# Kernel optimization log

Measured on AMD Instinct MI355X. Metric: run time of the kernel, lower is better.

## Reference

```python
import jax, jax.numpy as jnp
import numpy as np


def _nearest(img, cy, cx):
    # PyTorch F.grid_sample(mode='nearest', align_corners=False, padding_mode='zeros').
    # img: [B,C,H,W]; cy,cx: [B,N] normalized coords in [-1,1] (cy->H axis, cx->W axis).
    B, C, H, W = img.shape
    iy = jnp.rint((cy + 1.0) * H / 2.0 - 0.5)  # unnormalize then nearbyint
    ix = jnp.rint((cx + 1.0) * W / 2.0 - 0.5)
    valid = (iy >= 0) & (iy < H) & (ix >= 0) & (ix < W)
    flat = (jnp.clip(iy, 0, H - 1).astype(jnp.int32) * W
            + jnp.clip(ix, 0, W - 1).astype(jnp.int32))  # [B,N]
    g = jnp.take_along_axis(img.reshape(B, C, H * W), flat[:, None, :], axis=2)  # [B,C,N]
    g = jnp.where(valid[:, None, :], g, 0.0)
    return g.transpose(0, 2, 1)  # [B,N,C]


def setup_inputs() -> dict:
    key = jax.random.key(0)
    ks = jax.random.split(key, 16)
    B, N = 2, 16384
    h, w = 64, 64       # LR feat / lr_guide resolution
    H, W = 256, 256     # HR guide resolution
    Cf, Cg = 128, 128   # feat_dim, guide_dim
    inp = {
        'feat': jax.random.normal(ks[0], (B, Cf, h, w), jnp.float32),
        'coord': jax.random.uniform(ks[1], (B, N, 2), jnp.float32) * 2.0 - 1.0,
        'hr_guide': jax.random.normal(ks[2], (B, Cg, H, W), jnp.float32),
        'lr_guide': jax.random.normal(ks[3], (B, Cg, h, w), jnp.float32),
    }
    dims = [386, 1024, 512, 256, 128, 2]  # imnet_in_dim -> hidden_list -> out_dim
    for i in range(5):
        fan_in, fan_out = dims[i], dims[i + 1]
        scale = np.sqrt(2.0 / fan_in).astype(np.float32)
        inp[f'W{i}'] = jax.random.normal(ks[4 + i], (fan_out, fan_in), jnp.float32) * scale
        inp[f'b{i}'] = jnp.zeros((fan_out,), jnp.float32)
    return inp


def reference(feat, coord, hr_guide, lr_guide, W0, b0, W1, b1, W2, b2, W3, b3, W4, b4):
    b, c, h, w = feat.shape
    # make_coord((h,w), flatten=False).permute(2,0,1): channel 0 = y (h axis), 1 = x (w axis)
    ys = -1.0 + 2.0 * (jnp.arange(h, dtype=jnp.float32) + 0.5) / h
    xs = -1.0 + 2.0 * (jnp.arange(w, dtype=jnp.float32) + 0.5) / w
    fc = jnp.stack([jnp.broadcast_to(ys[:, None], (h, w)),
                    jnp.broadcast_to(xs[None, :], (h, w))], 0)[None]  # [1,2,h,w]
    fc = jnp.broadcast_to(fc, (b, 2, h, w))

    # coord.flip(-1) as grid -> grid x = coord[...,1] (W axis), grid y = coord[...,0] (H axis)
    q_guide_hr = _nearest(hr_guide, coord[..., 0], coord[..., 1])  # [B,N,Cg]

    # 4 offsets (vx,vy) in [-1,1]x[-1,1], scaled by rx=1/h, ry=1/w (loop order of torch code)
    offs = jnp.array([[-1., -1.], [-1., 1.], [1., -1.], [1., 1.]], jnp.float32)
    offs = offs * jnp.array([1.0 / h, 1.0 / w], jnp.float32)
    cK = coord[None] + offs[:, None, None, :]  # [4,B,N,2]

    samp = jax.vmap(_nearest, in_axes=(None, 0, 0))
    q_feat = samp(feat, cK[..., 0], cK[..., 1])      # [4,B,N,Cf]
    q_coord = samp(fc, cK[..., 0], cK[..., 1])       # [4,B,N,2]
    q_lr = samp(lr_guide, cK[..., 0], cK[..., 1])    # [4,B,N,Cg]

    rel = (coord[None] - q_coord) * jnp.array([float(h), float(w)], jnp.float32)  # [4,B,N,2]
    qg_hr = jnp.broadcast_to(q_guide_hr[None], q_lr.shape)
    inp = jnp.concatenate([q_feat, qg_hr, qg_hr - q_lr, rel], axis=-1)  # [4,B,N,386]

    x = inp
    for Wl, bl in ((W0, b0), (W1, b1), (W2, b2), (W3, b3)):
        x = jax.nn.relu(x @ Wl.T + bl)
    preds = x @ W4.T + b4                      # [4,B,N,2]
    preds = jnp.moveaxis(preds, 0, -1)         # [B,N,2,4]
    wgt = jax.nn.softmax(preds[:, :, 1, :], axis=-1)
    return jnp.sum(preds[:, :, 0, :] * wgt, axis=-1, keepdims=True)  # [B,N,1]
```

## Files before the change

### kernel.cpp

```cpp
#include <hip/hip_runtime.h>
#include <cstdint>

typedef __attribute__((ext_vector_type(8))) _Float16 half8;
typedef __attribute__((ext_vector_type(16))) float   f32x16;

#define BN 2
#define NN 16384
#define FH 64
#define FW 64
#define GH 256
#define GW 256
#define CC 128
#define M_TOTAL (4*BN*NN)
#define MROWS 64
#define NBLK (M_TOTAL/MROWS)

#define SX  456
#define SC  264
#define S2H 520
#define S3  264
#define S4  136
#define OFF_HC 29184
#define OFF_H3 33280
#define LDS_ELEMS 50176

#define MFMA(a,b,c) __builtin_amdgcn_mfma_f32_32x32x16_f16((a),(b),(c),0,0,0)

static __device__ __forceinline__ f32x16 zero16() {
  f32x16 z;
#pragma unroll
  for (int i = 0; i < 16; ++i) z[i] = 0.f;
  return z;
}
static __device__ __forceinline__ half8 zero8() {
  half8 z;
#pragma unroll
  for (int e = 0; e < 8; ++e) z[e] = (_Float16)0.f;
  return z;
}

__global__ void pack_w(const float* __restrict__ wsrc, _Float16* __restrict__ out,
                       int NT, int K, int KT) {
  int idx = blockIdx.x * 256 + threadIdx.x;
  int total = NT * KT * 64;
  if (idx >= total) return;
  int l = idx & 63;
  int t = idx >> 6;
  int kt = t % KT;
  int jt = t / KT;
  int row = jt * 32 + (l & 31);
  int k0 = kt * 16 + (l >> 5) * 8;
  _Float16* o = out + (size_t)idx * 8;
#pragma unroll
  for (int e = 0; e < 8; ++e) {
    int k = k0 + e;
    float v = (k < K) ? wsrc[(size_t)row * K + k] : 0.f;
    o[e] = (_Float16)v;
  }
}

__global__ void transpose_to_hwc(const float* __restrict__ in, _Float16* __restrict__ out,
                                 int C, int HH, int WW) {
  __shared__ float tile[32][33];
  const int xt = blockIdx.x, ct = blockIdx.y;
  const int bb = blockIdx.z / HH, y = blockIdx.z % HH;
  const int tx = threadIdx.x, ty = threadIdx.y;
  const int x0 = xt * 32, c0 = ct * 32;
#pragma unroll
  for (int i = 0; i < 4; ++i) {
    int c = c0 + ty + i * 8;
    tile[ty + i * 8][tx] = in[((size_t)(bb * C + c) * HH + y) * WW + x0 + tx];
  }
  __syncthreads();
#pragma unroll
  for (int i = 0; i < 4; ++i) {
    int x = x0 + ty + i * 8;
    out[((size_t)(bb * HH + y) * WW + x) * C + c0 + tx] = (_Float16)tile[tx][ty + i * 8];
  }
}

template<bool RELU>
static __device__ __forceinline__ void store_tile(const f32x16 acc, _Float16* lout, int ldo,
                                                  int row0, int col0,
                                                  const float* __restrict__ biasBase, int lane) {
  const int m = row0 + (lane & 31);
  const int s4 = (lane >> 5) * 4;
  _Float16* rp = lout + (size_t)m * ldo + col0 + s4;
  const float* bp = biasBase + s4;
#pragma unroll
  for (int g = 0; g < 4; ++g) {
    float4 bv = *(const float4*)(bp + 8 * g);
    union { _Float16 h[4]; unsigned long long u; } pk;
#pragma unroll
    for (int e = 0; e < 4; ++e) {
      float v = acc[4 * g + e] + ((const float*)&bv)[e];
      if (RELU) v = fmaxf(v, 0.f);
      pk.h[e] = (_Float16)v;
    }
    *(unsigned long long*)(rp + 8 * g) = pk.u;
  }
}

__global__ __launch_bounds__(512, 2) void jiif_main(
    const float* __restrict__ coord,
    const _Float16* __restrict__ featT, const _Float16* __restrict__ hrT,
    const _Float16* __restrict__ lrT,
    const _Float16* __restrict__ W0p, const _Float16* __restrict__ W1p,
    const _Float16* __restrict__ W2p, const _Float16* __restrict__ W3p,
    const float* __restrict__ b0, const float* __restrict__ b1,
    const float* __restrict__ b2, const float* __restrict__ b3,
    const float* __restrict__ W4, const float* __restrict__ b4,
    float* __restrict__ preds) {
  extern __shared__ _Float16 lds[];
  const int tid = threadIdx.x;
  const int w = tid >> 6, lane = tid & 63;
  const int m0 = blockIdx.x * MROWS;
  _Float16* X   = lds;
  _Float16* Hc  = lds + OFF_HC;
  _Float16* H2r = lds;
  _Float16* H3r = lds + OFF_H3;
  _Float16* H4r = lds;

  {
    const int r = tid >> 3;
    const int g = tid & 7;
    const int row = m0 + r;
    const int n = row & (NN - 1);
    const int bb = (row >> 14) & (BN - 1);
    const int k = row >> 15;
    const float c0 = coord[((size_t)bb * NN + n) * 2 + 0];
    const float c1 = coord[((size_t)bb * NN + n) * 2 + 1];
    const float cy = c0 + ((k < 2) ? -1.f : 1.f) * (1.f / FH);
    const float cx = c1 + ((k & 1) ? 1.f : -1.f) * (1.f / FW);
    const float fy = rintf((cy + 1.f) * (FH * 0.5f) - 0.5f);
    const float fx = rintf((cx + 1.f) * (FW * 0.5f) - 0.5f);
    const bool vF = (fy >= 0.f) && (fy < (float)FH) && (fx >= 0.f) && (fx < (float)FW);
    const int iy = max(0, min(FH - 1, (int)fy));
    const int ix = max(0, min(FW - 1, (int)fx));
    const float gy = rintf((c0 + 1.f) * (GH * 0.5f) - 0.5f);
    const float gx = rintf((c1 + 1.f) * (GW * 0.5f) - 0.5f);
    const bool vH = (gy >= 0.f) && (gy < (float)GH) && (gx >= 0.f) && (gx < (float)GW);
    const int jy = max(0, min(GH - 1, (int)gy));
    const int jx = max(0, min(GW - 1, (int)gx));
    const _Float16* fp = featT + (size_t)((bb * FH + iy) * FW + ix) * CC;
    const _Float16* lp = lrT  + (size_t)((bb * FH + iy) * FW + ix) * CC;
    const _Float16* hp = hrT  + (size_t)((bb * GH + jy) * GW + jx) * CC;
    _Float16* xr = X + (size_t)r * SX;
#pragma unroll
    for (int t = 0; t < 2; ++t) {
      const int c8 = g * 16 + t * 8;
      half8 fv = vF ? *(const half8*)(fp + c8) : zero8();
      half8 lv = vF ? *(const half8*)(lp + c8) : zero8();
      half8 hv = vH ? *(const half8*)(hp + c8) : zero8();
      *(half8*)(xr + c8) = fv;
      *(half8*)(xr + CC + c8) = hv;
      half8 dv = hv - lv;
      *(half8*)(xr + 2 * CC + c8) = dv;
    }
    *(unsigned long long*)(xr + 384 + g * 8) = 0ull;
    *(unsigned long long*)(xr + 384 + g * 8 + 4) = 0ull;
    if (g == 0) {
      const float qc0 = vF ? (-1.f + (float)(2 * iy + 1) * (1.f / FH)) : 0.f;
      const float qc1 = vF ? (-1.f + (float)(2 * ix + 1) * (1.f / FW)) : 0.f;
      xr[384] = (_Float16)((c0 - qc0) * (float)FH);
      xr[385] = (_Float16)((c1 - qc1) * (float)FW);
    }
  }
  __syncthreads();

  const int m31 = lane & 31;
  const int s8 = (lane >> 5) * 8;
  const _Float16* xb0 = X + (size_t)m31 * SX + s8;
  const _Float16* xb1 = X + (size_t)(32 + m31) * SX + s8;

  f32x16 a2_00 = zero16(), a2_01 = zero16(), a2_10 = zero16(), a2_11 = zero16();
#pragma unroll 1
  for (int c = 0; c < 4; ++c) {
    f32x16 a0lo = zero16(), a0hi = zero16();
    {
      const _Float16* wb = W0p + ((size_t)(c * 8 + w) * 28 * 64 + lane) * 8;
#pragma unroll 1
      for (int t = 0; t < 4; ++t) {
        half8 A[7], B0[7], B1[7];
#pragma unroll
        for (int i = 0; i < 7; ++i) {
          const int kt = t * 7 + i;
          A[i]  = *(const half8*)(wb + kt * 512);
          B0[i] = *(const half8*)(xb0 + kt * 16);
          B1[i] = *(const half8*)(xb1 + kt * 16);
        }
        __builtin_amdgcn_s_setprio(1);
#pragma unroll
        for (int i = 0; i < 7; ++i) {
          a0lo = MFMA(A[i], B0[i], a0lo);
          a0hi = MFMA(A[i], B1[i], a0hi);
        }
        __builtin_amdgcn_s_setprio(0);
      }
    }
    store_tile<true>(a0lo, Hc, SC, 0,  w * 32, b0 + c * 256 + w * 32, lane);
    store_tile<true>(a0hi, Hc, SC, 32, w * 32, b0 + c * 256 + w * 32, lane);
    __syncthreads();
    {
      const _Float16* w1a = W1p + ((size_t)(w * 64 + c * 16) * 64 + lane) * 8;
      const _Float16* w1b = W1p + ((size_t)((w + 8) * 64 + c * 16) * 64 + lane) * 8;
      const _Float16* hb0 = Hc + (size_t)m31 * SC + s8;
      const _Float16* hb1 = Hc + (size_t)(32 + m31) * SC + s8;
#pragma unroll 1
      for (int t = 0; t < 4; ++t) {
        half8 A0[4], A1[4], B0[4], B1[4];
#pragma unroll
        for (int i = 0; i < 4; ++i) {
          const int kt = t * 4 + i;
          A0[i] = *(const half8*)(w1a + kt * 512);
          A1[i] = *(const half8*)(w1b + kt * 512);
          B0[i] = *(const half8*)(hb0 + kt * 16);
          B1[i] = *(const half8*)(hb1 + kt * 16);
        }
        __builtin_amdgcn_s_setprio(1);
#pragma unroll
        for (int i = 0; i < 4; ++i) {
          a2_00 = MFMA(A0[i], B0[i], a2_00);
          a2_01 = MFMA(A0[i], B1[i], a2_01);
          a2_10 = MFMA(A1[i], B0[i], a2_10);
          a2_11 = MFMA(A1[i], B1[i], a2_11);
        }
        __builtin_amdgcn_s_setprio(0);
      }
    }
    __syncthreads();
  }

  store_tile<true>(a2_00, H2r, S2H, 0,  w * 32,       b1 + w * 32,       lane);
  store_tile<true>(a2_01, H2r, S2H, 32, w * 32,       b1 + w * 32,       lane);
  store_tile<true>(a2_10, H2r, S2H, 0,  256 + w * 32, b1 + 256 + w * 32, lane);
  store_tile<true>(a2_11, H2r, S2H, 32, 256 + w * 32, b1 + 256 + w * 32, lane);
  __syncthreads();

  {
    f32x16 a3lo = zero16(), a3hi = zero16();
    const _Float16* wb = W2p + ((size_t)(w * 32) * 64 + lane) * 8;
    const _Float16* hb0 = H2r + (size_t)m31 * S2H + s8;
    const _Float16* hb1 = H2r + (size_t)(32 + m31) * S2H + s8;
#pragma unroll 1
    for (int t = 0; t < 4; ++t) {
      half8 A[8], B0[8], B1[8];
#pragma unroll
      for (int i = 0; i < 8; ++i) {
        const int kt = t * 8 + i;
        A[i]  = *(const half8*)(wb + kt * 512);
        B0[i] = *(const half8*)(hb0 + kt * 16);
        B1[i] = *(const half8*)(hb1 + kt * 16);
      }
      __builtin_amdgcn_s_setprio(1);
#pragma unroll
      for (int i = 0; i < 8; ++i) {
        a3lo = MFMA(A[i], B0[i], a3lo);
        a3hi = MFMA(A[i], B1[i], a3hi);
      }
      __builtin_amdgcn_s_setprio(0);
    }
    store_tile<true>(a3lo, H3r, S3, 0,  w * 32, b2 + w * 32, lane);
    store_tile<true>(a3hi, H3r, S3, 32, w * 32, b2 + w * 32, lane);
  }
  __syncthreads();

  {
    const int j3 = w & 3, mts = w >> 2;
    f32x16 a4 = zero16();
    const _Float16* wb = W3p + ((size_t)(j3 * 16) * 64 + lane) * 8;
    const _Float16* hb = H3r + (size_t)(mts * 32 + m31) * S3 + s8;
#pragma unroll 1
    for (int t = 0; t < 2; ++t) {
      half8 A[8], B[8];
#pragma unroll
      for (int i = 0; i < 8; ++i) {
        const int kt = t * 8 + i;
        A[i] = *(const half8*)(wb + kt * 512);
        B[i] = *(const half8*)(hb + kt * 16);
      }
      __builtin_amdgcn_s_setprio(1);
#pragma unroll
      for (int i = 0; i < 8; ++i) a4 = MFMA(A[i], B[i], a4);
      __builtin_amdgcn_s_setprio(0);
    }
    store_tile<true>(a4, H4r, S4, mts * 32, j3 * 32, b3 + j3 * 32, lane);
  }
  __syncthreads();

  {
    const int m = tid >> 3;
    const int sub = tid & 7;
    const int j = sub & 1;
    const int q = sub >> 1;
    const _Float16* h4 = H4r + (size_t)m * S4 + q * 32;
    const float* w4 = W4 + j * CC + q * 32;
    float s = 0.f;
#pragma unroll
    for (int cc = 0; cc < 32; ++cc) s += (float)h4[cc] * w4[cc];
    s += __shfl_xor(s, 2);
    s += __shfl_xor(s, 4);
    if (q == 0) preds[(size_t)(m0 + m) * 2 + j] = s + b4[j];
  }
}

__global__ void jiif_combine(const float* __restrict__ preds, float* __restrict__ out) {
  const int i = blockIdx.x * 256 + threadIdx.x;
  if (i >= BN * NN) return;
  float p0[4], p1[4];
#pragma unroll
  for (int k = 0; k < 4; ++k) {
    p0[k] = preds[((size_t)k * BN * NN + i) * 2 + 0];
    p1[k] = preds[((size_t)k * BN * NN + i) * 2 + 1];
  }
  float mx = fmaxf(fmaxf(p1[0], p1[1]), fmaxf(p1[2], p1[3]));
  float se = 0.f, so = 0.f;
#pragma unroll
  for (int k = 0; k < 4; ++k) {
    float e = expf(p1[k] - mx);
    se += e;
    so += p0[k] * e;
  }
  out[i] = so / se;
}

extern "C" void kernel_launch(void* const* d_in, const int* in_sizes, int n_in,
                              void* d_out, int out_size, void* d_ws, size_t ws_size,
                              hipStream_t stream) {
  const float* feat  = (const float*)d_in[0];
  const float* coord = (const float*)d_in[1];
  const float* hr    = (const float*)d_in[2];
  const float* lr    = (const float*)d_in[3];
  const float* W0 = (const float*)d_in[4];  const float* b0 = (const float*)d_in[5];
  const float* W1 = (const float*)d_in[6];  const float* b1 = (const float*)d_in[7];
  const float* W2 = (const float*)d_in[8];  const float* b2 = (const float*)d_in[9];
  const float* W3 = (const float*)d_in[10]; const float* b3 = (const float*)d_in[11];
  const float* W4 = (const float*)d_in[12]; const float* b4 = (const float*)d_in[13];

  char* ws = (char*)d_ws;
  _Float16* W0p   = (_Float16*)(ws + 0);
  _Float16* W1p   = (_Float16*)(ws + 917504);
  _Float16* W2p   = (_Float16*)(ws + 1966080);
  _Float16* W3p   = (_Float16*)(ws + 2228224);
  _Float16* featT = (_Float16*)(ws + 2293760);
  _Float16* hrT   = (_Float16*)(ws + 4390912);
  _Float16* lrT   = (_Float16*)(ws + 37945344);
  float* preds    = (float*)(ws + 40042496);
  if (ws_size < 41091072) return;

  pack_w<<<224, 256, 0, stream>>>(W0, W0p, 32, 386, 28);
  pack_w<<<256, 256, 0, stream>>>(W1, W1p, 16, 1024, 64);
  pack_w<<<64,  256, 0, stream>>>(W2, W2p, 8, 512, 32);
  pack_w<<<16,  256, 0, stream>>>(W3, W3p, 4, 256, 16);

  transpose_to_hwc<<<dim3(2, 4, 128), dim3(32, 8), 0, stream>>>(feat, featT, CC, FH, FW);
  transpose_to_hwc<<<dim3(8, 4, 512), dim3(32, 8), 0, stream>>>(hr,   hrT,   CC, GH, GW);
  transpose_to_hwc<<<dim3(2, 4, 128), dim3(32, 8), 0, stream>>>(lr,   lrT,   CC, FH, FW);

  (void)hipFuncSetAttribute((const void*)jiif_main,
                            hipFuncAttributeMaxDynamicSharedMemorySize, LDS_ELEMS * 2);
  jiif_main<<<NBLK, 512, LDS_ELEMS * 2, stream>>>(
      coord, featT, hrT, lrT, W0p, W1p, W2p, W3p, b0, b1, b2, b3, W4, b4, preds);

  jiif_combine<<<(BN * NN + 255) / 256, 256, 0, stream>>>(preds, (float*)d_out);
}
```

Measured before the change: 373.1 us.

## Double-buffer operand loads across MFMA chunks with sched barriers in all GEMM layers

Replaces the per-chunk load-then-compute loops in each MLP layer with fully unrolled ping-pong register buffers. The next chunk's weight (global) and activation (LDS) fragments load while the current chunk's MFMAs run, and sched_barrier keeps the compiler from reordering them. The goal is to hide global and LDS load latency behind matrix math. In exchange it holds two buffer sets in registers, which raises VGPR pressure and may lower occupancy.

```diff
diff --git a/kernel.cpp b/kernel.cpp
--- a/kernel.cpp
+++ b/kernel.cpp
@@ -37,6 +37,76 @@
 #pragma unroll
   for (int e = 0; e < 8; ++e) z[e] = (_Float16)0.f;
   return z;
+}
+
+
+static __device__ __forceinline__ void ld_ab2(half8 (&A)[4], half8 (&B0)[4], half8 (&B1)[4],
+    const _Float16* wb, const _Float16* xb0, const _Float16* xb1, int t) {
+#pragma unroll
+  for (int i = 0; i < 4; ++i) {
+    const int kt = t * 4 + i;
+    A[i]  = *(const half8*)(wb  + kt * 512);
+    B0[i] = *(const half8*)(xb0 + kt * 16);
+    B1[i] = *(const half8*)(xb1 + kt * 16);
+  }
+}
+static __device__ __forceinline__ void mm_ab2(f32x16& lo, f32x16& hi,
+    const half8 (&A)[4], const half8 (&B0)[4], const half8 (&B1)[4]) {
+  __builtin_amdgcn_sched_barrier(0);
+  __builtin_amdgcn_s_setprio(1);
+#pragma unroll
+  for (int i = 0; i < 4; ++i) {
+    lo = MFMA(A[i], B0[i], lo);
+    hi = MFMA(A[i], B1[i], hi);
+  }
+  __builtin_amdgcn_s_setprio(0);
+  __builtin_amdgcn_sched_barrier(0);
+}
+
+static __device__ __forceinline__ void ld_a2b2(half8 (&A0)[4], half8 (&A1)[4],
+    half8 (&B0)[4], half8 (&B1)[4],
+    const _Float16* wa, const _Float16* wb, const _Float16* xb0, const _Float16* xb1, int t) {
+#pragma unroll
+  for (int i = 0; i < 4; ++i) {
+    const int kt = t * 4 + i;
+    A0[i] = *(const half8*)(wa + kt * 512);
+    A1[i] = *(const half8*)(wb + kt * 512);
+    B0[i] = *(const half8*)(xb0 + kt * 16);
+    B1[i] = *(const half8*)(xb1 + kt * 16);
+  }
+}
+static __device__ __forceinline__ void mm_a2b2(f32x16& a00, f32x16& a01, f32x16& a10, f32x16& a11,
+    const half8 (&A0)[4], const half8 (&A1)[4], const half8 (&B0)[4], const half8 (&B1)[4]) {
+  __builtin_amdgcn_sched_barrier(0);
+  __builtin_amdgcn_s_setprio(1);
+#pragma unroll
+  for (int i = 0; i < 4; ++i) {
+    a00 = MFMA(A0[i], B0[i], a00);
+    a01 = MFMA(A0[i], B1[i], a01);
+    a10 = MFMA(A1[i], B0[i], a10);
+    a11 = MFMA(A1[i], B1[i], a11);
+  }
+  __builtin_amdgcn_s_setprio(0);
+  __builtin_amdgcn_sched_barrier(0);
+}
+
+static __device__ __forceinline__ void ld_ab1(half8 (&A)[4], half8 (&B)[4],
+    const _Float16* wb, const _Float16* xb, int t) {
+#pragma unroll
+  for (int i = 0; i < 4; ++i) {
+    const int kt = t * 4 + i;
+    A[i] = *(const half8*)(wb + kt * 512);
+    B[i] = *(const half8*)(xb + kt * 16);
+  }
+}
+static __device__ __forceinline__ void mm_ab1(f32x16& acc,
+    const half8 (&A)[4], const half8 (&B)[4]) {
+  __builtin_amdgcn_sched_barrier(0);
+  __builtin_amdgcn_s_setprio(1);
+#pragma unroll
+  for (int i = 0; i < 4; ++i) acc = MFMA(A[i], B[i], acc);
+  __builtin_amdgcn_s_setprio(0);
+  __builtin_amdgcn_sched_barrier(0);
 }
 
 __global__ void pack_w(const float* __restrict__ wsrc, _Float16* __restrict__ out,
@@ -179,24 +249,15 @@
     f32x16 a0lo = zero16(), a0hi = zero16();
     {
       const _Float16* wb = W0p + ((size_t)(c * 8 + w) * 28 * 64 + lane) * 8;
-#pragma unroll 1
-      for (int t = 0; t < 4; ++t) {
-        half8 A[7], B0[7], B1[7];
-#pragma unroll
-        for (int i = 0; i < 7; ++i) {
-          const int kt = t * 7 + i;
-          A[i]  = *(const half8*)(wb + kt * 512);
-          B0[i] = *(const half8*)(xb0 + kt * 16);
-          B1[i] = *(const half8*)(xb1 + kt * 16);
-        }
-        __builtin_amdgcn_s_setprio(1);
-#pragma unroll
-        for (int i = 0; i < 7; ++i) {
-          a0lo = MFMA(A[i], B0[i], a0lo);
-          a0hi = MFMA(A[i], B1[i], a0hi);
-        }
-        __builtin_amdgcn_s_setprio(0);
-      }
+      half8 sA[4], sB0[4], sB1[4], tA[4], tB0[4], tB1[4];
+      ld_ab2(sA, sB0, sB1, wb, xb0, xb1, 0);
+      ld_ab2(tA, tB0, tB1, wb, xb0, xb1, 1); mm_ab2(a0lo, a0hi, sA, sB0, sB1);
+      ld_ab2(sA, sB0, sB1, wb, xb0, xb1, 2); mm_ab2(a0lo, a0hi, tA, tB0, tB1);
+      ld_ab2(tA, tB0, tB1, wb, xb0, xb1, 3); mm_ab2(a0lo, a0hi, sA, sB0, sB1);
+      ld_ab2(sA, sB0, sB1, wb, xb0, xb1, 4); mm_ab2(a0lo, a0hi, tA, tB0, tB1);
+      ld_ab2(tA, tB0, tB1, wb, xb0, xb1, 5); mm_ab2(a0lo, a0hi, sA, sB0, sB1);
+      ld_ab2(sA, sB0, sB1, wb, xb0, xb1, 6); mm_ab2(a0lo, a0hi, tA, tB0, tB1);
+      mm_ab2(a0lo, a0hi, sA, sB0, sB1);
     }
     store_tile<true>(a0lo, Hc, SC, 0,  w * 32, b0 + c * 256 + w * 32, lane);
     store_tile<true>(a0hi, Hc, SC, 32, w * 32, b0 + c * 256 + w * 32, lane);
@@ -206,27 +267,15 @@
       const _Float16* w1b = W1p + ((size_t)((w + 8) * 64 + c * 16) * 64 + lane) * 8;
       const _Float16* hb0 = Hc + (size_t)m31 * SC + s8;
       const _Float16* hb1 = Hc + (size_t)(32 + m31) * SC + s8;
-#pragma unroll 1
-      for (int t = 0; t < 4; ++t) {
-        half8 A0[4], A1[4], B0[4], B1[4];
-#pragma unroll
-        for (int i = 0; i < 4; ++i) {
-          const int kt = t * 4 + i;
-          A0[i] = *(const half8*)(w1a + kt * 512);
-          A1[i] = *(const half8*)(w1b + kt * 512);
-          B0[i] = *(const half8*)(hb0 + kt * 16);
-          B1[i] = *(const half8*)(hb1 + kt * 16);
-        }
-        __builtin_amdgcn_s_setprio(1);
-#pragma unroll
-        for (int i = 0; i < 4; ++i) {
-          a2_00 = MFMA(A0[i], B0[i], a2_00);
-          a2_01 = MFMA(A0[i], B1[i], a2_01);
-          a2_10 = MFMA(A1[i], B0[i], a2_10);
-          a2_11 = MFMA(A1[i], B1[i], a2_11);
-        }
-        __builtin_amdgcn_s_setprio(0);
-      }
+      half8 sA0[4], sA1[4], sB0[4], sB1[4], tA0[4], tA1[4], tB0[4], tB1[4];
+      ld_a2b2(sA0, sA1, sB0, sB1, w1a, w1b, hb0, hb1, 0);
+      ld_a2b2(tA0, tA1, tB0, tB1, w1a, w1b, hb0, hb1, 1);
+      mm_a2b2(a2_00, a2_01, a2_10, a2_11, sA0, sA1, sB0, sB1);
+      ld_a2b2(sA0, sA1, sB0, sB1, w1a, w1b, hb0, hb1, 2);
+      mm_a2b2(a2_00, a2_01, a2_10, a2_11, tA0, tA1, tB0, tB1);
+      ld_a2b2(tA0, tA1, tB0, tB1, w1a, w1b, hb0, hb1, 3);
+      mm_a2b2(a2_00, a2_01, a2_10, a2_11, sA0, sA1, sB0, sB1);
+      mm_a2b2(a2_00, a2_01, a2_10, a2_11, tA0, tA1, tB0, tB1);
     }
     __syncthreads();
   }
@@ -242,24 +291,16 @@
     const _Float16* wb = W2p + ((size_t)(w * 32) * 64 + lane) * 8;
     const _Float16* hb0 = H2r + (size_t)m31 * S2H + s8;
     const _Float16* hb1 = H2r + (size_t)(32 + m31) * S2H + s8;
-#pragma unroll 1
-    for (int t = 0; t < 4; ++t) {
-      half8 A[8], B0[8], B1[8];
-#pragma unroll
-      for (int i = 0; i < 8; ++i) {
-        const int kt = t * 8 + i;
-        A[i]  = *(const half8*)(wb + kt * 512);
-        B0[i] = *(const half8*)(hb0 + kt * 16);
-        B1[i] = *(const half8*)(hb1 + kt * 16);
-      }
-      __builtin_amdgcn_s_setprio(1);
-#pragma unroll
-      for (int i = 0; i < 8; ++i) {
-        a3lo = MFMA(A[i], B0[i], a3lo);
-        a3hi = MFMA(A[i], B1[i], a3hi);
-      }
-      __builtin_amdgcn_s_setprio(0);
-    }
+    half8 sA[4], sB0[4], sB1[4], tA[4], tB0[4], tB1[4];
+    ld_ab2(sA, sB0, sB1, wb, hb0, hb1, 0);
+    ld_ab2(tA, tB0, tB1, wb, hb0, hb1, 1); mm_ab2(a3lo, a3hi, sA, sB0, sB1);
+    ld_ab2(sA, sB0, sB1, wb, hb0, hb1, 2); mm_ab2(a3lo, a3hi, tA, tB0, tB1);
+    ld_ab2(tA, tB0, tB1, wb, hb0, hb1, 3); mm_ab2(a3lo, a3hi, sA, sB0, sB1);
+    ld_ab2(sA, sB0, sB1, wb, hb0, hb1, 4); mm_ab2(a3lo, a3hi, tA, tB0, tB1);
+    ld_ab2(tA, tB0, tB1, wb, hb0, hb1, 5); mm_ab2(a3lo, a3hi, sA, sB0, sB1);
+    ld_ab2(sA, sB0, sB1, wb, hb0, hb1, 6); mm_ab2(a3lo, a3hi, tA, tB0, tB1);
+    ld_ab2(tA, tB0, tB1, wb, hb0, hb1, 7); mm_ab2(a3lo, a3hi, sA, sB0, sB1);
+    mm_ab2(a3lo, a3hi, tA, tB0, tB1);
     store_tile<true>(a3lo, H3r, S3, 0,  w * 32, b2 + w * 32, lane);
     store_tile<true>(a3hi, H3r, S3, 32, w * 32, b2 + w * 32, lane);
   }
@@ -270,20 +311,12 @@
     f32x16 a4 = zero16();
     const _Float16* wb = W3p + ((size_t)(j3 * 16) * 64 + lane) * 8;
     const _Float16* hb = H3r + (size_t)(mts * 32 + m31) * S3 + s8;
-#pragma unroll 1
-    for (int t = 0; t < 2; ++t) {
-      half8 A[8], B[8];
-#pragma unroll
-      for (int i = 0; i < 8; ++i) {
-        const int kt = t * 8 + i;
-        A[i] = *(const half8*)(wb + kt * 512);
-        B[i] = *(const half8*)(hb + kt * 16);
-      }
-      __builtin_amdgcn_s_setprio(1);
-#pragma unroll
-      for (int i = 0; i < 8; ++i) a4 = MFMA(A[i], B[i], a4);
-      __builtin_amdgcn_s_setprio(0);
-    }
+    half8 sA[4], sB[4], tA[4], tB[4];
+    ld_ab1(sA, sB, wb, hb, 0);
+    ld_ab1(tA, tB, wb, hb, 1); mm_ab1(a4, sA, sB);
+    ld_ab1(sA, sB, wb, hb, 2); mm_ab1(a4, tA, tB);
+    ld_ab1(tA, tB, wb, hb, 3); mm_ab1(a4, sA, sB);
+    mm_ab1(a4, tA, tB);
     store_tile<true>(a4, H4r, S4, mts * 32, j3 * 32, b3 + j3 * 32, lane);
   }
   __syncthreads();
```

Measured after the change: 359.4 us. 3.7% less time.

## Restructure layer0/1 into two 512-wide chunks with double-buffered register prefetch

Applied to the files above, without the earlier changes.

Layer 0 is now computed in two halves of 512 hidden units, each stored to a widened LDS buffer, instead of four 256-wide chunks. Layer 1 therefore accumulates over two large K chunks, which halves the number of block barriers. All GEMM loops now use ping-pong register buffers, so the next K-slice is loaded while the MFMAs run on the current one, with sched_barrier fencing the MFMA groups. The cost is a larger LDS footprint (about 159KB) and more registers, which may reduce occupancy.

```diff
diff --git a/kernel.cpp b/kernel.cpp
--- a/kernel.cpp
+++ b/kernel.cpp
@@ -16,13 +16,13 @@
 #define NBLK (M_TOTAL/MROWS)
 
 #define SX  456
-#define SC  264
+#define SHC 520
 #define S2H 520
 #define S3  264
 #define S4  136
 #define OFF_HC 29184
-#define OFF_H3 33280
-#define LDS_ELEMS 50176
+#define OFF_H3 62464
+#define LDS_ELEMS 79360
 
 #define MFMA(a,b,c) __builtin_amdgcn_mfma_f32_32x32x16_f16((a),(b),(c),0,0,0)
 
@@ -37,6 +37,76 @@
 #pragma unroll
   for (int e = 0; e < 8; ++e) z[e] = (_Float16)0.f;
   return z;
+}
+
+template<int NB>
+static __device__ __forceinline__ void ldA2(half8 (&A0)[NB], half8 (&A1)[NB],
+    const _Float16* wa, const _Float16* wb, int t) {
+#pragma unroll
+  for (int i = 0; i < NB; ++i) {
+    const int kt = t * NB + i;
+    A0[i] = *(const half8*)(wa + kt * 512);
+    A1[i] = *(const half8*)(wb + kt * 512);
+  }
+}
+template<int NB>
+static __device__ __forceinline__ void ldA1(half8 (&A)[NB], const _Float16* wa, int t) {
+#pragma unroll
+  for (int i = 0; i < NB; ++i) A[i] = *(const half8*)(wa + (t * NB + i) * 512);
+}
+template<int NB>
+static __device__ __forceinline__ void ldB2(half8 (&B0)[NB], half8 (&B1)[NB],
+    const _Float16* p0, const _Float16* p1, int t) {
+#pragma unroll
+  for (int i = 0; i < NB; ++i) {
+    const int kt = t * NB + i;
+    B0[i] = *(const half8*)(p0 + kt * 16);
+    B1[i] = *(const half8*)(p1 + kt * 16);
+  }
+}
+template<int NB>
+static __device__ __forceinline__ void ldB1(half8 (&B)[NB], const _Float16* p, int t) {
+#pragma unroll
+  for (int i = 0; i < NB; ++i) B[i] = *(const half8*)(p + (t * NB + i) * 16);
+}
+
+template<int NB>
+static __device__ __forceinline__ void mm_22(f32x16& a00, f32x16& a01, f32x16& a10, f32x16& a11,
+    const half8 (&A0)[NB], const half8 (&A1)[NB], const half8 (&B0)[NB], const half8 (&B1)[NB]) {
+  __builtin_amdgcn_sched_barrier(0);
+  __builtin_amdgcn_s_setprio(1);
+#pragma unroll
+  for (int i = 0; i < NB; ++i) {
+    a00 = MFMA(A0[i], B0[i], a00);
+    a01 = MFMA(A0[i], B1[i], a01);
+    a10 = MFMA(A1[i], B0[i], a10);
+    a11 = MFMA(A1[i], B1[i], a11);
+  }
+  __builtin_amdgcn_s_setprio(0);
+  __builtin_amdgcn_sched_barrier(0);
+}
+template<int NB>
+static __device__ __forceinline__ void mm_12(f32x16& lo, f32x16& hi,
+    const half8 (&A)[NB], const half8 (&B0)[NB], const half8 (&B1)[NB]) {
+  __builtin_amdgcn_sched_barrier(0);
+  __builtin_amdgcn_s_setprio(1);
+#pragma unroll
+  for (int i = 0; i < NB; ++i) {
+    lo = MFMA(A[i], B0[i], lo);
+    hi = MFMA(A[i], B1[i], hi);
+  }
+  __builtin_amdgcn_s_setprio(0);
+  __builtin_amdgcn_sched_barrier(0);
+}
+template<int NB>
+static __device__ __forceinline__ void mm_11(f32x16& acc,
+    const half8 (&A)[NB], const half8 (&B)[NB]) {
+  __builtin_amdgcn_sched_barrier(0);
+  __builtin_amdgcn_s_setprio(1);
+#pragma unroll
+  for (int i = 0; i < NB; ++i) acc = MFMA(A[i], B[i], acc);
+  __builtin_amdgcn_s_setprio(0);
+  __builtin_amdgcn_sched_barrier(0);
 }
 
 __global__ void pack_w(const float* __restrict__ wsrc, _Float16* __restrict__ out,
@@ -171,95 +241,116 @@
   const int m31 = lane & 31;
   const int s8 = (lane >> 5) * 8;
   const _Float16* xb0 = X + (size_t)m31 * SX + s8;
-  const _Float16* xb1 = X + (size_t)(32 + m31) * SX + s8;
+  const _Float16* xb1 = xb0 + 32 * SX;
+  const _Float16* hb0 = Hc + (size_t)m31 * SHC + s8;
+  const _Float16* hb1 = hb0 + 32 * SHC;
+
+  {
+    f32x16 a00 = zero16(), a01 = zero16(), a10 = zero16(), a11 = zero16();
+    const _Float16* wa = W0p + ((size_t)(2 * w) * 28 * 64 + lane) * 8;
+    const _Float16* wb = wa + 28 * 512;
+    half8 pA0[2], pA1[2], pB0[2], pB1[2], qA0[2], qA1[2], qB0[2], qB1[2];
+    ldA2<2>(pA0, pA1, wa, wb, 0); ldB2<2>(pB0, pB1, xb0, xb1, 0);
+    ldA2<2>(qA0, qA1, wa, wb, 1); ldB2<2>(qB0, qB1, xb0, xb1, 1);
+#pragma unroll 1
+    for (int u = 0; u < 6; ++u) {
+      mm_22<2>(a00, a01, a10, a11, pA0, pA1, pB0, pB1);
+      ldA2<2>(pA0, pA1, wa, wb, 2 * u + 2); ldB2<2>(pB0, pB1, xb0, xb1, 2 * u + 2);
+      mm_22<2>(a00, a01, a10, a11, qA0, qA1, qB0, qB1);
+      ldA2<2>(qA0, qA1, wa, wb, 2 * u + 3); ldB2<2>(qB0, qB1, xb0, xb1, 2 * u + 3);
+    }
+    mm_22<2>(a00, a01, a10, a11, pA0, pA1, pB0, pB1);
+    mm_22<2>(a00, a01, a10, a11, qA0, qA1, qB0, qB1);
+    store_tile<true>(a00, Hc, SHC, 0,  (2 * w) * 32,     b0 + (2 * w) * 32,     lane);
+    store_tile<true>(a01, Hc, SHC, 32, (2 * w) * 32,     b0 + (2 * w) * 32,     lane);
+    store_tile<true>(a10, Hc, SHC, 0,  (2 * w + 1) * 32, b0 + (2 * w + 1) * 32, lane);
+    store_tile<true>(a11, Hc, SHC, 32, (2 * w + 1) * 32, b0 + (2 * w + 1) * 32, lane);
+  }
+  __syncthreads();
 
   f32x16 a2_00 = zero16(), a2_01 = zero16(), a2_10 = zero16(), a2_11 = zero16();
+  const _Float16* w1a = W1p + ((size_t)(2 * w) * 64 * 64 + lane) * 8;
+  const _Float16* w1b = w1a + 64 * 512;
+  {
+    half8 sA0[4], sA1[4], sB0[4], sB1[4], tA0[4], tA1[4], tB0[4], tB1[4];
+    ldA2<4>(sA0, sA1, w1a, w1b, 0); ldB2<4>(sB0, sB1, hb0, hb1, 0);
+    ldA2<4>(tA0, tA1, w1a, w1b, 1); ldB2<4>(tB0, tB1, hb0, hb1, 1);
 #pragma unroll 1
-  for (int c = 0; c < 4; ++c) {
-    f32x16 a0lo = zero16(), a0hi = zero16();
-    {
-      const _Float16* wb = W0p + ((size_t)(c * 8 + w) * 28 * 64 + lane) * 8;
+    for (int u = 0; u < 3; ++u) {
+      mm_22<4>(a2_00, a2_01, a2_10, a2_11, sA0, sA1, sB0, sB1);
+      ldA2<4>(sA0, sA1, w1a, w1b, 2 * u + 2); ldB2<4>(sB0, sB1, hb0, hb1, 2 * u + 2);
+      mm_22<4>(a2_00, a2_01, a2_10, a2_11, tA0, tA1, tB0, tB1);
+      ldA2<4>(tA0, tA1, w1a, w1b, 2 * u + 3); ldB2<4>(tB0, tB1, hb0, hb1, 2 * u + 3);
+    }
+    mm_22<4>(a2_00, a2_01, a2_10, a2_11, sA0, sA1, sB0, sB1);
+    mm_22<4>(a2_00, a2_01, a2_10, a2_11, tA0, tA1, tB0, tB1);
+  }
+  __syncthreads();
+
+  {
+    f32x16 a00 = zero16(), a01 = zero16(), a10 = zero16(), a11 = zero16();
+    const _Float16* wa = W0p + ((size_t)(16 + 2 * w) * 28 * 64 + lane) * 8;
+    const _Float16* wb = wa + 28 * 512;
+    half8 pA0[2], pA1[2], pB0[2], pB1[2], qA0[2], qA1[2], qB0[2], qB1[2];
+    ldA2<2>(pA0, pA1, wa, wb, 0); ldB2<2>(pB0, pB1, xb0, xb1, 0);
+    ldA2<2>(qA0, qA1, wa, wb, 1); ldB2<2>(qB0, qB1, xb0, xb1, 1);
 #pragma unroll 1
-      for (int t = 0; t < 4; ++t) {
-        half8 A[7], B0[7], B1[7];
-#pragma unroll
-        for (int i = 0; i < 7; ++i) {
-          const int kt = t * 7 + i;
-          A[i]  = *(const half8*)(wb + kt * 512);
-          B0[i] = *(const half8*)(xb0 + kt * 16);
-          B1[i] = *(const half8*)(xb1 + kt * 16);
-        }
-        __builtin_amdgcn_s_setprio(1);
-#pragma unroll
-        for (int i = 0; i < 7; ++i) {
-          a0lo = MFMA(A[i], B0[i], a0lo);
-          a0hi = MFMA(A[i], B1[i], a0hi);
-        }
-        __builtin_amdgcn_s_setprio(0);
-      }
-    }
-    store_tile<true>(a0lo, Hc, SC, 0,  w * 32, b0 + c * 256 + w * 32, lane);
-    store_tile<true>(a0hi, Hc, SC, 32, w * 32, b0 + c * 256 + w * 32, lane);
-    __syncthreads();
-    {
-      const _Float16* w1a = W1p + ((size_t)(w * 64 + c * 16) * 64 + lane) * 8;
-      const _Float16* w1b = W1p + ((size_t)((w + 8) * 64 + c * 16) * 64 + lane) * 8;
-      const _Float16* hb0 = Hc + (size_t)m31 * SC + s8;
-      const _Float16* hb1 = Hc + (size_t)(32 + m31) * SC + s8;
+    for (int u = 0; u < 6; ++u) {
+      mm_22<2>(a00, a01, a10, a11, pA0, pA1, pB0, pB1);
+      ldA2<2>(pA0, pA1, wa, wb, 2 * u + 2); ldB2<2>(pB0, pB1, xb0, xb1, 2 * u + 2);
+      mm_22<2>(a00, a01, a10, a11, qA0, qA1, qB0, qB1);
+      ldA2<2>(qA0, qA1, wa, wb, 2 * u + 3); ldB2<2>(qB0, qB1, xb0, xb1, 2 * u + 3);
+    }
+    mm_22<2>(a00, a01, a10, a11, pA0, pA1, pB0, pB1);
+    mm_22<2>(a00, a01, a10, a11, qA0, qA1, qB0, qB1);
+    store_tile<true>(a00, Hc, SHC, 0,  (2 * w) * 32,     b0 + 512 + (2 * w) * 32,     lane);
+    store_tile<true>(a01, Hc, SHC, 32, (2 * w) * 32,     b0 + 512 + (2 * w) * 32,     lane);
+    store_tile<true>(a10, Hc, SHC, 0,  (2 * w + 1) * 32, b0 + 512 + (2 * w + 1) * 32, lane);
+    store_tile<true>(a11, Hc, SHC, 32, (2 * w + 1) * 32, b0 + 512 + (2 * w + 1) * 32, lane);
+  }
+  __syncthreads();
+
+  {
+    const _Float16* wa = w1a + 32 * 512;
+    const _Float16* wb = w1b + 32 * 512;
+    half8 sA0[4], sA1[4], sB0[4], sB1[4], tA0[4], tA1[4], tB0[4], tB1[4];
+    ldA2<4>(sA0, sA1, wa, wb, 0); ldB2<4>(sB0, sB1, hb0, hb1, 0);
+    ldA2<4>(tA0, tA1, wa, wb, 1); ldB2<4>(tB0, tB1, hb0, hb1, 1);
 #pragma unroll 1
-      for (int t = 0; t < 4; ++t) {
-        half8 A0[4], A1[4], B0[4], B1[4];
-#pragma unroll
-        for (int i = 0; i < 4; ++i) {
-          const int kt = t * 4 + i;
-          A0[i] = *(const half8*)(w1a + kt * 512);
-          A1[i] = *(const half8*)(w1b + kt * 512);
-          B0[i] = *(const half8*)(hb0 + kt * 16);
-          B1[i] = *(const half8*)(hb1 + kt * 16);
-        }
-        __builtin_amdgcn_s_setprio(1);
-#pragma unroll
-        for (int i = 0; i < 4; ++i) {
-          a2_00 = MFMA(A0[i], B0[i], a2_00);
-          a2_01 = MFMA(A0[i], B1[i], a2_01);
-          a2_10 = MFMA(A1[i], B0[i], a2_10);
-          a2_11 = MFMA(A1[i], B1[i], a2_11);
-        }
-        __builtin_amdgcn_s_setprio(0);
-      }
-    }
-    __syncthreads();
-  }
-
-  store_tile<true>(a2_00, H2r, S2H, 0,  w * 32,       b1 + w * 32,       lane);
-  store_tile<true>(a2_01, H2r, S2H, 32, w * 32,       b1 + w * 32,       lane);
-  store_tile<true>(a2_10, H2r, S2H, 0,  256 + w * 32, b1 + 256 + w * 32, lane);
-  store_tile<true>(a2_11, H2r, S2H, 32, 256 + w * 32, b1 + 256 + w * 32, lane);
-  __syncthreads();
-
-  {
+    for (int u = 0; u < 3; ++u) {
+      mm_22<4>(a2_00, a2_01, a2_10, a2_11, sA0, sA1, sB0, sB1);
+      ldA2<4>(sA0, sA1, wa, wb, 2 * u + 2); ldB2<4>(sB0, sB1, hb0, hb1, 2 * u + 2);
+      mm_22<4>(a2_00, a2_01, a2_10, a2_11, tA0, tA1, tB0, tB1);
+      ldA2<4>(tA0, tA1, wa, wb, 2 * u + 3); ldB2<4>(tB0, tB1, hb0, hb1, 2 * u + 3);
+    }
+    mm_22<4>(a2_00, a2_01, a2_10, a2_11, sA0, sA1, sB0, sB1);
+    mm_22<4>(a2_00, a2_01, a2_10, a2_11, tA0, tA1, tB0, tB1);
+  }
+  __syncthreads();
+
+  store_tile<true>(a2_00, H2r, S2H, 0,  (2 * w) * 32,     b1 + (2 * w) * 32,     lane);
+  store_tile<true>(a2_01, H2r, S2H, 32, (2 * w) * 32,     b1 + (2 * w) * 32,     lane);
+  store_tile<true>(a2_10, H2r, S2H, 0,  (2 * w + 1) * 32, b1 + (2 * w + 1) * 32, lane);
+  store_tile<true>(a2_11, H2r, S2H, 32, (2 * w + 1) * 32, b1 + (2 * w + 1) * 32, lane);
+  __syncthreads();
+
+  {
+    const _Float16* wb2 = W2p + ((size_t)w * 32 * 64 + lane) * 8;
+    const _Float16* h2b0 = H2r + (size_t)m31 * S2H + s8;
+    const _Float16* h2b1 = h2b0 + 32 * S2H;
     f32x16 a3lo = zero16(), a3hi = zero16();
-    const _Float16* wb = W2p + ((size_t)(w * 32) * 64 + lane) * 8;
-    const _Float16* hb0 = H2r + (size_t)m31 * S2H + s8;
-    const _Float16* hb1 = H2r + (size_t)(32 + m31) * S2H + s8;
+    half8 sA[4], sB0[4], sB1[4], tA[4], tB0[4], tB1[4];
+    ldA1<4>(sA, wb2, 0); ldB2<4>(sB0, sB1, h2b0, h2b1, 0);
+    ldA1<4>(tA, wb2, 1); ldB2<4>(tB0, tB1, h2b0, h2b1, 1);
 #pragma unroll 1
-    for (int t = 0; t < 4; ++t) {
-      half8 A[8], B0[8], B1[8];
-#pragma unroll
-      for (int i = 0; i < 8; ++i) {
-        const int kt = t * 8 + i;
-        A[i]  = *(const half8*)(wb + kt * 512);
-        B0[i] = *(const half8*)(hb0 + kt * 16);
-        B1[i] = *(const half8*)(hb1 + kt * 16);
-      }
-      __builtin_amdgcn_s_setprio(1);
-#pragma unroll
-      for (int i = 0; i < 8; ++i) {
-        a3lo = MFMA(A[i], B0[i], a3lo);
-        a3hi = MFMA(A[i], B1[i], a3hi);
-      }
-      __builtin_amdgcn_s_setprio(0);
-    }
+    for (int u = 0; u < 3; ++u) {
+      mm_12<4>(a3lo, a3hi, sA, sB0, sB1);
+      ldA1<4>(sA, wb2, 2 * u + 2); ldB2<4>(sB0, sB1, h2b0, h2b1, 2 * u + 2);
+      mm_12<4>(a3lo, a3hi, tA, tB0, tB1);
+      ldA1<4>(tA, wb2, 2 * u + 3); ldB2<4>(tB0, tB1, h2b0, h2b1, 2 * u + 3);
+    }
+    mm_12<4>(a3lo, a3hi, sA, sB0, sB1);
+    mm_12<4>(a3lo, a3hi, tA, tB0, tB1);
     store_tile<true>(a3lo, H3r, S3, 0,  w * 32, b2 + w * 32, lane);
     store_tile<true>(a3hi, H3r, S3, 32, w * 32, b2 + w * 32, lane);
   }
@@ -267,23 +358,18 @@
 
   {
     const int j3 = w & 3, mts = w >> 2;
+    const _Float16* wb3 = W3p + ((size_t)j3 * 16 * 64 + lane) * 8;
+    const _Float16* h3b = H3r + (size_t)(mts * 32 + m31) * S3 + s8;
     f32x16 a4 = zero16();
-    const _Float16* wb = W3p + ((size_t)(j3 * 16) * 64 + lane) * 8;
-    const _Float16* hb = H3r + (size_t)(mts * 32 + m31) * S3 + s8;
-#pragma unroll 1
-    for (int t = 0; t < 2; ++t) {
-      half8 A[8], B[8];
-#pragma unroll
-      for (int i = 0; i < 8; ++i) {
-        const int kt = t * 8 + i;
-        A[i] = *(const half8*)(wb + kt * 512);
-        B[i] = *(const half8*)(hb + kt * 16);
-      }
-      __builtin_amdgcn_s_setprio(1);
-#pragma unroll
-      for (int i = 0; i < 8; ++i) a4 = MFMA(A[i], B[i], a4);
-      __builtin_amdgcn_s_setprio(0);
-    }
+    half8 sA[4], sB[4], tA[4], tB[4];
+    ldA1<4>(sA, wb3, 0); ldB1<4>(sB, h3b, 0);
+    ldA1<4>(tA, wb3, 1); ldB1<4>(tB, h3b, 1);
+    mm_11<4>(a4, sA, sB);
+    ldA1<4>(sA, wb3, 2); ldB1<4>(sB, h3b, 2);
+    mm_11<4>(a4, tA, tB);
+    ldA1<4>(tA, wb3, 3); ldB1<4>(tB, h3b, 3);
+    mm_11<4>(a4, sA, sB);
+    mm_11<4>(a4, tA, tB);
     store_tile<true>(a4, H4r, S4, mts * 32, j3 * 32, b3 + j3 * 32, lane);
   }
   __syncthreads();
```

Measured after the change: 946.0 us. +153.6%, slower.
